# Optimization experiments

Hardware: AMD Instinct MI355X
Metric: run time of the kernel (lower is better)

Reference implementation:

```python
import jax, jax.numpy as jnp
import numpy as np

EPS = 1e-5
N_KNN = 16


def _knn_idx(query_feat, ref_feat, k):
    # query_feat: (B, N, C), ref_feat: (B, M, C) -> idx (B, N, k) of smallest sq-dist
    q2 = jnp.sum(query_feat * query_feat, axis=-1, keepdims=True)        # (B,N,1)
    r2 = jnp.sum(ref_feat * ref_feat, axis=-1)[:, None, :]               # (B,1,M)
    d = q2 + r2 - 2.0 * jnp.einsum('bnc,bmc->bnm', query_feat, ref_feat)  # (B,N,M)
    _, idx = jax.lax.top_k(-d, k)
    return idx


def _group(x, idx):
    # x: (B, C, M), idx: (B, N, k) -> (B, C, N, k)
    B, C, M = x.shape
    _, N, k = idx.shape
    flat = jnp.broadcast_to(idx.reshape(B, 1, N * k), (B, C, N * k))
    return jnp.take_along_axis(x, flat, axis=2).reshape(B, C, N, k)


def _bn(x, g, b, m, v):
    # eval-mode BatchNorm2d over channel axis 1 of (B,C,N,k)
    inv = g / jnp.sqrt(v + EPS)
    return x * inv[None, :, None, None] + (b - m * inv)[None, :, None, None]


def setup_inputs() -> dict:
    key = jax.random.key(0)
    ks = jax.random.split(key, 24)
    B, C, N, N2 = 4, 256, 2048, 2048
    ph = 64  # pos_hidden_dim
    ah = 256  # dim * attn_hidden_multiplier = 64*4
    s = lambda fan: 1.0 / np.sqrt(fan)
    inp = {
        'pcd': jax.random.normal(ks[0], (B, 3, N), jnp.float32),
        'feat': jax.random.normal(ks[1], (B, C, N), jnp.float32),
        'pcd_feadb': jax.random.normal(ks[2], (B, 3, N2), jnp.float32),
        'feat_feadb': jax.random.normal(ks[3], (B, C, N2), jnp.float32),
        'pos_w1': jax.random.normal(ks[4], (ph, 3), jnp.float32) * s(3),
        'pos_b1': jax.random.normal(ks[5], (ph,), jnp.float32) * 0.01,
        'pos_g': jax.random.uniform(ks[6], (ph,), jnp.float32, 0.5, 1.5),
        'pos_be': jax.random.normal(ks[7], (ph,), jnp.float32) * 0.01,
        'pos_m': jax.random.normal(ks[8], (ph,), jnp.float32) * 0.1,
        'pos_v': jax.random.uniform(ks[9], (ph,), jnp.float32, 0.5, 1.5),
        'pos_w2': jax.random.normal(ks[10], (C, ph), jnp.float32) * s(ph),
        'pos_b2': jax.random.normal(ks[11], (C,), jnp.float32) * 0.01,
        'attn_w1': jax.random.normal(ks[12], (ah, C), jnp.float32) * s(C),
        'attn_b1': jax.random.normal(ks[13], (ah,), jnp.float32) * 0.01,
        'attn_g': jax.random.uniform(ks[14], (ah,), jnp.float32, 0.5, 1.5),
        'attn_be': jax.random.normal(ks[15], (ah,), jnp.float32) * 0.01,
        'attn_m': jax.random.normal(ks[16], (ah,), jnp.float32) * 0.1,
        'attn_v': jax.random.uniform(ks[17], (ah,), jnp.float32, 0.5, 1.5),
        'attn_w2': jax.random.normal(ks[18], (C, ah), jnp.float32) * s(ah),
        'attn_b2': jax.random.normal(ks[19], (C,), jnp.float32) * 0.01,
    }
    return inp


def reference(pcd, feat, pcd_feadb, feat_feadb,
              pos_w1, pos_b1, pos_g, pos_be, pos_m, pos_v, pos_w2, pos_b2,
              attn_w1, attn_b1, attn_g, attn_be, attn_m, attn_v, attn_w2, attn_b2):
    fusion_pcd = jnp.concatenate([pcd, pcd_feadb], axis=2)    # (B,3,M)
    fusion_feat = jnp.concatenate([feat, feat_feadb], axis=2)  # (B,C,M)
    # KNN in feature space: neighbors of each key point among fusion set
    idx = _knn_idx(jnp.swapaxes(feat, 1, 2), jnp.swapaxes(fusion_feat, 1, 2), N_KNN)  # (B,N,k)
    group_point = _group(fusion_pcd, idx)   # (B,3,N,k)
    group_feat = _group(fusion_feat, idx)   # (B,C,N,k)
    qk_rel = feat[:, :, :, None] - group_feat
    pos_rel = pcd[:, :, :, None] - group_point
    # pos_mlp: conv1x1 -> BN -> relu -> conv1x1
    h = jnp.einsum('oc,bcnk->bonk', pos_w1, pos_rel) + pos_b1[None, :, None, None]
    h = jax.nn.relu(_bn(h, pos_g, pos_be, pos_m, pos_v))
    pos_embedding = jnp.einsum('oc,bcnk->bonk', pos_w2, h) + pos_b2[None, :, None, None]
    # attn_mlp
    a = jnp.einsum('oc,bcnk->bonk', attn_w1, qk_rel + pos_embedding) + attn_b1[None, :, None, None]
    a = jax.nn.relu(_bn(a, attn_g, attn_be, attn_m, attn_v))
    a = jnp.einsum('oc,bcnk->bonk', attn_w2, a) + attn_b2[None, :, None, None]
    sample_weight = jax.nn.softmax(a, axis=-1)  # softmax over the k neighbors
    refined_feat = jnp.sum(sample_weight * (group_feat + pos_embedding), axis=-1)  # (B,C,N)
    return refined_feat
```

## Files before the change

### kernel.cpp

```cpp
#include <hip/hip_runtime.h>
#include <float.h>

#define CDIM 256
#define NPTS 2048
#define MPTS 4096
#define NB   4
#define KNN  16
#define COLS 64
#define NCHUNK 8
#define CSIZE  512
#define NSTEPS 16
#define QPB   128

typedef _Float16 half8 __attribute__((ext_vector_type(8)));
typedef _Float16 half4 __attribute__((ext_vector_type(4)));
typedef float    f32x4 __attribute__((ext_vector_type(4)));

__device__ __forceinline__ int swzS(int row, int byte) {
    return row * 512 + (byte ^ ((row & 7) << 4));
}
__device__ __forceinline__ int swz128(int row, int byte) {
    return row * 128 + (byte ^ ((row & 7) << 4));
}

__device__ __forceinline__ float sum16(float v) {
    v += __uint_as_float(__builtin_amdgcn_update_dpp(0, __float_as_uint(v), 0x128, 0xF, 0xF, true));
    v += __uint_as_float(__builtin_amdgcn_update_dpp(0, __float_as_uint(v), 0x124, 0xF, 0xF, true));
    v += __uint_as_float(__builtin_amdgcn_update_dpp(0, __float_as_uint(v), 0x122, 0xF, 0xF, true));
    v += __uint_as_float(__builtin_amdgcn_update_dpp(0, __float_as_uint(v), 0x121, 0xF, 0xF, true));
    return v;
}

#define CEA(x, y)                                                               \
    { unsigned lo_ = kk[x] < kk[y] ? kk[x] : kk[y];                             \
      unsigned hi_ = kk[x] < kk[y] ? kk[y] : kk[x];                             \
      kk[x] = lo_; kk[y] = hi_; }
#define CED(x, y)                                                               \
    { unsigned hi_ = td[x] > td[y] ? td[x] : td[y];                             \
      unsigned lo_ = td[x] > td[y] ? td[y] : td[x];                             \
      td[x] = hi_; td[y] = lo_; }
#define RESORT16                                                                \
    CED(0,8) CED(1,9) CED(2,10) CED(3,11) CED(4,12) CED(5,13) CED(6,14) CED(7,15) \
    CED(0,4) CED(1,5) CED(2,6) CED(3,7) CED(8,12) CED(9,13) CED(10,14) CED(11,15) \
    CED(0,2) CED(1,3) CED(4,6) CED(5,7) CED(8,10) CED(9,11) CED(12,14) CED(13,15) \
    CED(0,1) CED(2,3) CED(4,5) CED(6,7) CED(8,9) CED(10,11) CED(12,13) CED(14,15)

__global__ __launch_bounds__(256) void tposeHL2(const float* __restrict__ feat,
                                                const float* __restrict__ featdb,
                                                _Float16* __restrict__ featH,
                                                _Float16* __restrict__ featL,
                                                float* __restrict__ r2) {
    __shared__ float red[8][33];
    const int b = blockIdx.y;
    const int mt = blockIdx.x;
    const int m = threadIdx.x & 31;
    const int cp = threadIdx.x >> 5;
    const int mg = mt * 32 + m;
    const float* src = (mg < NPTS) ? (feat + (size_t)b * CDIM * NPTS + mg)
                                   : (featdb + (size_t)b * CDIM * NPTS + (mg - NPTS));
    const int c0 = cp * 32;
    float acc = 0.f;
    half8 hh[4], ll[4];
#pragma unroll
    for (int i = 0; i < 32; i++) {
        float v = src[(size_t)(c0 + i) * NPTS];
        acc += v * v;
        _Float16 h = (_Float16)v;
        hh[i >> 3][i & 7] = h;
        ll[i >> 3][i & 7] = (_Float16)(v - (float)h);
    }
    _Float16* dh = featH + ((size_t)b * MPTS + mg) * CDIM + c0;
    _Float16* dl = featL + ((size_t)b * MPTS + mg) * CDIM + c0;
#pragma unroll
    for (int i = 0; i < 4; i++) {
        *(half8*)(dh + i * 8) = hh[i];
        *(half8*)(dl + i * 8) = ll[i];
    }
    red[cp][m] = acc;
    __syncthreads();
    if (threadIdx.x < 32) {
        float s = 0.f;
#pragma unroll
        for (int j = 0; j < 8; j++) s += red[j][threadIdx.x];
        r2[b * MPTS + mt * 32 + threadIdx.x] = s;
    }
}

__global__ __launch_bounds__(256) void wcvt(const float* __restrict__ aw1,
                                            const float* __restrict__ aw2,
                                            const float* __restrict__ pw2,
                                            _Float16* __restrict__ aw1h,
                                            _Float16* __restrict__ aw2h,
                                            _Float16* __restrict__ pw2h) {
    int i = blockIdx.x * 256 + threadIdx.x;
    if (i < 65536) { aw1h[i] = (_Float16)aw1[i]; aw2h[i] = (_Float16)aw2[i]; }
    if (i < 16384) { pw2h[i] = (_Float16)pw2[i]; }
}

__global__ __launch_bounds__(512, 4) void score_knn(const _Float16* __restrict__ featH,
                                                    const _Float16* __restrict__ featL,
                                                    const float* __restrict__ r2g,
                                                    unsigned* __restrict__ partial) {
    __shared__ __align__(16) char sbuf[65536];
    __shared__ float sr2[CSIZE];

    const int tid = threadIdx.x;
    const int lane = tid & 63, wave = tid >> 6;
    const int l15 = lane & 15, l4 = lane >> 4;
    const int chunk = blockIdx.x, qt = blockIdx.y, b = blockIdx.z;
    const int nq = qt * QPB + wave * 16 + l15;
    const int m0 = chunk * CSIZE;

    sr2[tid] = r2g[b * MPTS + m0 + tid];

    half8 qh[8], ql[8];
    {
        const _Float16* qb = featH + ((size_t)b * MPTS + nq) * CDIM + l4 * 8;
        const _Float16* qL = featL + ((size_t)b * MPTS + nq) * CDIM + l4 * 8;
#pragma unroll
        for (int ks = 0; ks < 8; ks++) {
            qh[ks] = *(const half8*)(qb + ks * 32);
            ql[ks] = *(const half8*)(qL + ks * 32);
        }
    }

    int adr[8];
#pragma unroll
    for (int ks = 0; ks < 8; ks++)
        adr[ks] = (ks * 4 + l4) * 512 + ((l15 * 16) ^ ((ks & 7) << 4));

    const int srow = tid >> 4;
    const int o0 = 2 * (tid & 15);
    int wadr[2];
#pragma unroll
    for (int j = 0; j < 2; j++) {
        int o = o0 + j;
        wadr[j] = o * 512 + ((srow * 16) ^ (((o >> 2) & 7) << 4));
    }
    const char* gH = (const char*)(featH + ((size_t)b * MPTS + m0 + srow) * CDIM) + o0 * 16;
    const char* gL = (const char*)(featL + ((size_t)b * MPTS + m0 + srow) * CDIM) + o0 * 16;

    unsigned td[16];
#pragma unroll
    for (int i = 0; i < 16; i++) td[i] = 0xFFFFFFFFu;

    half8 pH[2], pL[2];
#pragma unroll
    for (int j = 0; j < 2; j++) {
        pH[j] = *(const half8*)(gH + j * 16);
        pL[j] = *(const half8*)(gL + j * 16);
    }
    gH += 32 * CDIM * 2;
    gL += 32 * CDIM * 2;

    for (int s = 0; s < NSTEPS; ++s) {
        char* buf = sbuf + (s & 1) * 32768;
#pragma unroll
        for (int j = 0; j < 2; j++) {
            *(half8*)(buf + wadr[j])         = pH[j];
            *(half8*)(buf + 16384 + wadr[j]) = pL[j];
        }
        __syncthreads();

        if (s < NSTEPS - 1) {
#pragma unroll
            for (int j = 0; j < 2; j++) {
                pH[j] = *(const half8*)(gH + j * 16);
                pL[j] = *(const half8*)(gL + j * 16);
            }
            gH += 32 * CDIM * 2;
            gL += 32 * CDIM * 2;
        }

        unsigned kk[8];
#pragma unroll
        for (int sub = 0; sub < 2; ++sub) {
            f32x4 a0 = {0.f, 0.f, 0.f, 0.f};
            f32x4 a1 = {0.f, 0.f, 0.f, 0.f};
            f32x4 a2 = {0.f, 0.f, 0.f, 0.f};
#pragma unroll
            for (int ks = 0; ks < 8; ks++) {
                half8 ah = *(const half8*)(buf + adr[ks] + sub * 256);
                half8 al = *(const half8*)(buf + 16384 + adr[ks] + sub * 256);
                a0 = __builtin_amdgcn_mfma_f32_16x16x32_f16(ah, qh[ks], a0, 0, 0, 0);
                a1 = __builtin_amdgcn_mfma_f32_16x16x32_f16(ah, ql[ks], a1, 0, 0, 0);
                a2 = __builtin_amdgcn_mfma_f32_16x16x32_f16(al, qh[ks], a2, 0, 0, 0);
            }
            float4 s4 = *(const float4*)(sr2 + s * 32 + sub * 16 + 4 * l4);
            const float sv[4] = {s4.x, s4.y, s4.z, s4.w};
            const int mloc0 = s * 32 + sub * 16 + 4 * l4;
#pragma unroll
            for (int r = 0; r < 4; r++) {
                float d = fmaxf(sv[r] - 2.f * (a0[r] + a1[r] + a2[r]), 0.f);
                unsigned dq = (unsigned)(d * 4096.f);
                dq = dq > 0x7FFFF0u ? 0x7FFFF0u : dq;
                kk[sub * 4 + r] = (dq << 9) | (unsigned)(mloc0 + r);
            }
        }
        CEA(0,1) CEA(2,3) CEA(4,5) CEA(6,7)
        CEA(0,2) CEA(1,3) CEA(4,6) CEA(5,7)
        CEA(1,2) CEA(5,6) CEA(0,4) CEA(3,7)
        CEA(1,5) CEA(2,6)
        CEA(1,4) CEA(3,6)
        CEA(2,4) CEA(3,5)
        CEA(3,4)
#pragma unroll
        for (int i = 0; i < 8; i++) td[i] = td[i] < kk[i] ? td[i] : kk[i];
        RESORT16
    }

#pragma unroll
    for (int rr = 0; rr < 2; rr++) {
        const int dx = 16 << rr;
        unsigned ot[16];
#pragma unroll
        for (int e = 0; e < 16; e++) ot[e] = __shfl_xor(td[e], dx);
#pragma unroll
        for (int e = 0; e < 16; e++) {
            unsigned o = ot[15 - e];
            td[e] = td[e] < o ? td[e] : o;
        }
        RESORT16
    }
    if (l4 == 0) {
        const size_t qrow = (size_t)b * NPTS + qt * QPB + wave * 16 + l15;
#pragma unroll
        for (int e = 0; e < 16; e++)
            partial[(size_t)(chunk * 16 + e) * (NB * NPTS) + qrow] = td[e];
    }
}

__global__ __launch_bounds__(256) void merge16(const unsigned* __restrict__ partial,
                                               int* __restrict__ idxout) {
    const int row = blockIdx.x * 256 + threadIdx.x;
    unsigned long long td[16];
#pragma unroll
    for (int i = 0; i < 16; i++) td[i] = 0x8000000000ull + (unsigned long long)i;
    unsigned long long curmax = 0x800000000Full;
    for (int e = 0; e < NCHUNK * 16; e++) {
        unsigned k = partial[(size_t)e * (NB * NPTS) + row];
        unsigned long long k64 =
            (((unsigned long long)(k >> 9)) << 12) |
            (unsigned long long)((unsigned)((e >> 4) << 9) | (k & 0x1FFu));
        if (k64 < curmax) {
#pragma unroll
            for (int i_ = 0; i_ < 16; i_++) td[i_] = (td[i_] == curmax) ? k64 : td[i_];
            unsigned long long nm_ = td[0];
#pragma unroll
            for (int i_ = 1; i_ < 16; i_++) nm_ = td[i_] > nm_ ? td[i_] : nm_;
            curmax = nm_;
        }
    }
#pragma unroll
    for (int e = 0; e < 16; e++) idxout[row * 16 + e] = (int)(td[e] & 0xFFFull);
}

__global__ __launch_bounds__(512, 4) void fused_mlp6(
    const float* __restrict__ pcd, const float* __restrict__ pcddb,
    const _Float16* __restrict__ featH, const int* __restrict__ knn,
    const float* __restrict__ pw1, const float* __restrict__ pb1,
    const float* __restrict__ pg, const float* __restrict__ pbe,
    const float* __restrict__ pm, const float* __restrict__ pv,
    const _Float16* __restrict__ pw2h, const float* __restrict__ pb2,
    const _Float16* __restrict__ aw1h, const float* __restrict__ ab1,
    const float* __restrict__ ag, const float* __restrict__ abe,
    const float* __restrict__ am, const float* __restrict__ av,
    const _Float16* __restrict__ aw2h,
    float* __restrict__ out) {
    __shared__ __align__(16) _Float16 xbuf[COLS * 256];
    __shared__ __align__(16) _Float16 hbuf[COLS * 64];
    __shared__ __align__(16) float pr[3][COLS];
    __shared__ int sidx[COLS];
    __shared__ __align__(16) float ainv[256], ash2[256], pinv[64], psh[64];

    const int tid = threadIdx.x;
    const int lane = tid & 63, wave = tid >> 6;
    const int l15 = lane & 15, l4 = lane >> 4;
    const int blk = blockIdx.x;
    const int b = blk >> 9;
    const int n0 = (blk & 511) * 4;
    const int R0 = wave * 32;

    if (tid < COLS) {
        sidx[tid] = knn[(size_t)(b * NPTS + n0 + (tid >> 4)) * KNN + (tid & 15)];
    } else if (tid < COLS + 256) {
        int c = tid - COLS;
        float inv = ag[c] / sqrtf(av[c] + 1e-5f);
        ainv[c] = inv;
        ash2[c] = abe[c] - am[c] * inv + ab1[c] * inv;
    } else if (tid < COLS + 256 + 64) {
        int o = tid - COLS - 256;
        float inv = pg[o] / sqrtf(pv[o] + 1e-5f);
        pinv[o] = inv;
        psh[o] = pbe[o] - pm[o] * inv;
    }
    half8 wp[2][2];
#pragma unroll
    for (int rt = 0; rt < 2; rt++)
#pragma unroll
        for (int ks = 0; ks < 2; ks++)
            wp[rt][ks] = *(const half8*)(pw2h + (size_t)(R0 + rt * 16 + l15) * 64 +
                                         ks * 32 + l4 * 8);
    __syncthreads();

    if (tid < 3 * COLS) {
        int c = tid >> 6, col = tid & 63;
        int m = sidx[col];
        const float* pc = pcd + ((size_t)b * 3 + c) * NPTS;
        const float* px = pcddb + ((size_t)b * 3 + c) * NPTS;
        float gp = (m < NPTS) ? pc[m] : px[m - NPTS];
        pr[c][col] = pc[n0 + (col >> 4)] - gp;
    }
    const int colx = tid & 63;
    const int c0x = (tid >> 6) * 32;
    half8 fmv[4], fnv[4];
    {
        const _Float16* fmp = featH + ((size_t)b * MPTS + sidx[colx]) * CDIM + c0x;
        const _Float16* fnp = featH + ((size_t)b * MPTS + n0 + (colx >> 4)) * CDIM + c0x;
#pragma unroll
        for (int j = 0; j < 4; j++) {
            fmv[j] = *(const half8*)(fmp + j * 8);
            fnv[j] = *(const half8*)(fnp + j * 8);
        }
    }
    __syncthreads();

    {
        int col = tid >> 3, o0 = (tid & 7) * 8;
        float x0 = pr[0][col], x1 = pr[1][col], x2 = pr[2][col];
        half8 hv;
#pragma unroll
        for (int i = 0; i < 8; i++) {
            int o = o0 + i;
            float v = pw1[o * 3] * x0 + pw1[o * 3 + 1] * x1 + pw1[o * 3 + 2] * x2 + pb1[o];
            v = fmaxf(v * pinv[o] + psh[o], 0.f);
            hv[i] = (_Float16)v;
        }
        *(half8*)((char*)hbuf + swz128(col, o0 * 2)) = hv;
    }
    __syncthreads();

    f32x4 acc[2][4];
#pragma unroll
    for (int rt = 0; rt < 2; rt++)
#pragma unroll
        for (int ct = 0; ct < 4; ct++) acc[rt][ct] = (f32x4){0.f, 0.f, 0.f, 0.f};
#pragma unroll
    for (int ks = 0; ks < 2; ks++) {
        int k0 = ks * 32 + l4 * 8;
#pragma unroll
        for (int ct = 0; ct < 4; ct++) {
            half8 bb = *(const half8*)((char*)hbuf + swz128(ct * 16 + l15, k0 * 2));
            acc[0][ct] = __builtin_amdgcn_mfma_f32_16x16x32_f16(wp[0][ks], bb, acc[0][ct], 0, 0, 0);
            acc[1][ct] = __builtin_amdgcn_mfma_f32_16x16x32_f16(wp[1][ks], bb, acc[1][ct], 0, 0, 0);
        }
    }
    half4 pe4[2][4];
#pragma unroll
    for (int rt = 0; rt < 2; rt++) {
        int cb = R0 + rt * 16 + 4 * l4;
        float4 pb = *(const float4*)(pb2 + cb);
        float pbv[4] = {pb.x, pb.y, pb.z, pb.w};
#pragma unroll
        for (int ct = 0; ct < 4; ct++) {
            int col = ct * 16 + l15;
            half4 p4;
#pragma unroll
            for (int r = 0; r < 4; r++) p4[r] = (_Float16)(acc[rt][ct][r] + pbv[r]);
            pe4[rt][ct] = p4;
            *(half4*)((char*)xbuf + swzS(col, cb * 2)) = p4;
        }
    }
    __syncthreads();

#pragma unroll
    for (int j = 0; j < 4; j++) {
        int c = c0x + j * 8;
        half8 vp = *(const half8*)((char*)xbuf + swzS(colx, c * 2));
        half8 xv = fnv[j] - fmv[j] + vp;
        *(half8*)((char*)xbuf + swzS(colx, c * 2)) = xv;
    }
    half8 wa[8];
#pragma unroll
    for (int ks = 0; ks < 8; ks++)
        wa[ks] = *(const half8*)(aw1h + (size_t)(R0 + l15) * 256 + ks * 32 + l4 * 8);
    __syncthreads();

#pragma unroll
    for (int rt = 0; rt < 2; rt++)
#pragma unroll
        for (int ct = 0; ct < 4; ct++) acc[rt][ct] = (f32x4){0.f, 0.f, 0.f, 0.f};
#pragma unroll
    for (int ks = 0; ks < 8; ks++) {
        int k0 = ks * 32 + l4 * 8;
#pragma unroll
        for (int ct = 0; ct < 4; ct++) {
            half8 bb = *(const half8*)((char*)xbuf + swzS(ct * 16 + l15, k0 * 2));
            acc[0][ct] = __builtin_amdgcn_mfma_f32_16x16x32_f16(wa[ks], bb, acc[0][ct], 0, 0, 0);
        }
    }
#pragma unroll
    for (int ks = 0; ks < 8; ks++)
        wa[ks] = *(const half8*)(aw1h + (size_t)(R0 + 16 + l15) * 256 + ks * 32 + l4 * 8);
#pragma unroll
    for (int ks = 0; ks < 8; ks++) {
        int k0 = ks * 32 + l4 * 8;
#pragma unroll
        for (int ct = 0; ct < 4; ct++) {
            half8 bb = *(const half8*)((char*)xbuf + swzS(ct * 16 + l15, k0 * 2));
            acc[1][ct] = __builtin_amdgcn_mfma_f32_16x16x32_f16(wa[ks], bb, acc[1][ct], 0, 0, 0);
        }
    }
    __syncthreads();

#pragma unroll
    for (int rt = 0; rt < 2; rt++) {
        int cb = R0 + rt * 16 + 4 * l4;
        float4 iv = *(const float4*)(&ainv[cb]);
        float4 sh = *(const float4*)(&ash2[cb]);
        float ivv[4] = {iv.x, iv.y, iv.z, iv.w};
        float shv[4] = {sh.x, sh.y, sh.z, sh.w};
#pragma unroll
        for (int ct = 0; ct < 4; ct++) {
            int col = ct * 16 + l15;
            half4 h4;
#pragma unroll
            for (int r = 0; r < 4; r++)
                h4[r] = (_Float16)fmaxf(acc[rt][ct][r] * ivv[r] + shv[r], 0.f);
            *(half4*)((char*)xbuf + swzS(col, cb * 2)) = h4;
        }
    }
#pragma unroll
    for (int ks = 0; ks < 8; ks++)
        wa[ks] = *(const half8*)(aw2h + (size_t)(R0 + l15) * 256 + ks * 32 + l4 * 8);
    __syncthreads();

#pragma unroll
    for (int rt = 0; rt < 2; rt++)
#pragma unroll
        for (int ct = 0; ct < 4; ct++) acc[rt][ct] = (f32x4){0.f, 0.f, 0.f, 0.f};
#pragma unroll
    for (int ks = 0; ks < 8; ks++) {
        int k0 = ks * 32 + l4 * 8;
#pragma unroll
        for (int ct = 0; ct < 4; ct++) {
            half8 bb = *(const half8*)((char*)xbuf + swzS(ct * 16 + l15, k0 * 2));
            acc[0][ct] = __builtin_amdgcn_mfma_f32_16x16x32_f16(wa[ks], bb, acc[0][ct], 0, 0, 0);
        }
    }
#pragma unroll
    for (int ks = 0; ks < 8; ks++)
        wa[ks] = *(const half8*)(aw2h + (size_t)(R0 + 16 + l15) * 256 + ks * 32 + l4 * 8);
#pragma unroll
    for (int ks = 0; ks < 8; ks++) {
        int k0 = ks * 32 + l4 * 8;
#pragma unroll
        for (int ct = 0; ct < 4; ct++) {
            half8 bb = *(const half8*)((char*)xbuf + swzS(ct * 16 + l15, k0 * 2));
            acc[1][ct] = __builtin_amdgcn_mfma_f32_16x16x32_f16(wa[ks], bb, acc[1][ct], 0, 0, 0);
        }
    }

#pragma unroll
    for (int rt = 0; rt < 2; rt++) {
        int cb = R0 + rt * 16 + 4 * l4;
        half4 gfa[4];
#pragma unroll
        for (int ct = 0; ct < 4; ct++)
            gfa[ct] = *(const half4*)(featH +
                ((size_t)b * MPTS + sidx[ct * 16 + l15]) * CDIM + cb);
#pragma unroll
        for (int ct = 0; ct < 4; ct++) {
            float oo[4], ss[4];
#pragma unroll
            for (int r = 0; r < 4; r++) {
                float v = acc[rt][ct][r];
                v = fminf(fmaxf(v, -60.f), 60.f);
                float e = __expf(v);
                float sv = (float)gfa[ct][r] + (float)pe4[rt][ct][r];
                ss[r] = sum16(e);
                oo[r] = sum16(e * sv);
            }
            if (l15 < 4) {
                float o = l15 == 0 ? oo[0] : l15 == 1 ? oo[1] : l15 == 2 ? oo[2] : oo[3];
                float s = l15 == 0 ? ss[0] : l15 == 1 ? ss[1] : l15 == 2 ? ss[2] : ss[3];
                out[((size_t)b * CDIM + cb + l15) * NPTS + n0 + ct] =
                    o * __builtin_amdgcn_rcpf(s);
            }
        }
    }
}

extern "C" void kernel_launch(void* const* d_in, const int* in_sizes, int n_in,
                              void* d_out, int out_size, void* d_ws, size_t ws_size,
                              hipStream_t stream) {
    const float* pcd    = (const float*)d_in[0];
    const float* feat   = (const float*)d_in[1];
    const float* pcddb  = (const float*)d_in[2];
    const float* featdb = (const float*)d_in[3];
    const float* pw1 = (const float*)d_in[4];
    const float* pb1 = (const float*)d_in[5];
    const float* pg  = (const float*)d_in[6];
    const float* pbe = (const float*)d_in[7];
    const float* pm  = (const float*)d_in[8];
    const float* pv  = (const float*)d_in[9];
    const float* pw2 = (const float*)d_in[10];
    const float* pb2 = (const float*)d_in[11];
    const float* aw1 = (const float*)d_in[12];
    const float* ab1 = (const float*)d_in[13];
    const float* ag  = (const float*)d_in[14];
    const float* abe = (const float*)d_in[15];
    const float* am  = (const float*)d_in[16];
    const float* av  = (const float*)d_in[17];
    const float* aw2 = (const float*)d_in[18];
    float* out = (float*)d_out;

    char* ws = (char*)d_ws;
    _Float16* featH   = (_Float16*)(ws);
    _Float16* featL   = (_Float16*)(ws + 8388608);
    float*    ws_r2   = (float*)(ws + 16777216);
    unsigned* partial = (unsigned*)(ws + 16842752);
    int*      ws_idx  = (int*)(ws + 21037056);
    _Float16* aw1h    = (_Float16*)(ws + 21561344);
    _Float16* aw2h    = (_Float16*)(ws + 21692416);
    _Float16* pw2h    = (_Float16*)(ws + 21823488);

    wcvt<<<256, 256, 0, stream>>>(aw1, aw2, pw2, aw1h, aw2h, pw2h);
    tposeHL2<<<dim3(MPTS / 32, NB), 256, 0, stream>>>(feat, featdb, featH, featL, ws_r2);
    score_knn<<<dim3(NCHUNK, NPTS / QPB, NB), 512, 0, stream>>>(featH, featL, ws_r2, partial);
    merge16<<<NB * NPTS / 256, 256, 0, stream>>>(partial, ws_idx);
    fused_mlp6<<<NB * (NPTS / 4), 512, 0, stream>>>(
        pcd, pcddb, featH, ws_idx,
        pw1, pb1, pg, pbe, pm, pv, pw2h, pb2,
        aw1h, ab1, ag, abe, am, av, aw2h, out);
}
```

Baseline: 272.4 us.

## Double queries per score_knn block to halve reference-tile reloads

Raises queries per block from 128 to 256 and launches 1024-thread blocks, so each staged reference chunk in shared memory serves twice as many query waves. Each thread now loads one half8 per step instead of two, and the r2 shared-memory fill is guarded for the larger block. This halves the global reads of the reference features and the number of blocks. In exchange, fewer blocks fit per CU, each barrier has to sync 16 waves, and there are fewer blocks overall to fill the GPU.

After: 266.9 us. 2.0% less time.

```diff
diff --git a/kernel.cpp b/kernel.cpp
--- a/kernel.cpp
+++ b/kernel.cpp
@@ -10,7 +10,7 @@
 #define NCHUNK 8
 #define CSIZE  512
 #define NSTEPS 16
-#define QPB   128
+#define QPB   256
 
 typedef _Float16 half8 __attribute__((ext_vector_type(8)));
 typedef _Float16 half4 __attribute__((ext_vector_type(4)));
@@ -97,10 +97,10 @@
     if (i < 16384) { pw2h[i] = (_Float16)pw2[i]; }
 }
 
-__global__ __launch_bounds__(512, 4) void score_knn(const _Float16* __restrict__ featH,
-                                                    const _Float16* __restrict__ featL,
-                                                    const float* __restrict__ r2g,
-                                                    unsigned* __restrict__ partial) {
+__global__ __launch_bounds__(1024, 2) void score_knn(const _Float16* __restrict__ featH,
+                                                     const _Float16* __restrict__ featL,
+                                                     const float* __restrict__ r2g,
+                                                     unsigned* __restrict__ partial) {
     __shared__ __align__(16) char sbuf[65536];
     __shared__ float sr2[CSIZE];
 
@@ -111,7 +111,7 @@
     const int nq = qt * QPB + wave * 16 + l15;
     const int m0 = chunk * CSIZE;
 
-    sr2[tid] = r2g[b * MPTS + m0 + tid];
+    if (tid < CSIZE) sr2[tid] = r2g[b * MPTS + m0 + tid];
 
     half8 qh[8], ql[8];
     {
@@ -129,45 +129,30 @@
     for (int ks = 0; ks < 8; ks++)
         adr[ks] = (ks * 4 + l4) * 512 + ((l15 * 16) ^ ((ks & 7) << 4));
 
-    const int srow = tid >> 4;
-    const int o0 = 2 * (tid & 15);
-    int wadr[2];
-#pragma unroll
-    for (int j = 0; j < 2; j++) {
-        int o = o0 + j;
-        wadr[j] = o * 512 + ((srow * 16) ^ (((o >> 2) & 7) << 4));
-    }
-    const char* gH = (const char*)(featH + ((size_t)b * MPTS + m0 + srow) * CDIM) + o0 * 16;
-    const char* gL = (const char*)(featL + ((size_t)b * MPTS + m0 + srow) * CDIM) + o0 * 16;
+    const int srow = tid >> 5;
+    const int oo = tid & 31;
+    const int wadr = oo * 512 + ((srow * 16) ^ (((oo >> 2) & 7) << 4));
+    const char* gH = (const char*)(featH + ((size_t)b * MPTS + m0 + srow) * CDIM) + oo * 16;
+    const char* gL = (const char*)(featL + ((size_t)b * MPTS + m0 + srow) * CDIM) + oo * 16;
 
     unsigned td[16];
 #pragma unroll
     for (int i = 0; i < 16; i++) td[i] = 0xFFFFFFFFu;
 
-    half8 pH[2], pL[2];
-#pragma unroll
-    for (int j = 0; j < 2; j++) {
-        pH[j] = *(const half8*)(gH + j * 16);
-        pL[j] = *(const half8*)(gL + j * 16);
-    }
+    half8 pH = *(const half8*)gH;
+    half8 pL = *(const half8*)gL;
     gH += 32 * CDIM * 2;
     gL += 32 * CDIM * 2;
 
     for (int s = 0; s < NSTEPS; ++s) {
         char* buf = sbuf + (s & 1) * 32768;
-#pragma unroll
-        for (int j = 0; j < 2; j++) {
-            *(half8*)(buf + wadr[j])         = pH[j];
-            *(half8*)(buf + 16384 + wadr[j]) = pL[j];
-        }
+        *(half8*)(buf + wadr)         = pH;
+        *(half8*)(buf + 16384 + wadr) = pL;
         __syncthreads();
 
         if (s < NSTEPS - 1) {
-#pragma unroll
-            for (int j = 0; j < 2; j++) {
-                pH[j] = *(const half8*)(gH + j * 16);
-                pL[j] = *(const half8*)(gL + j * 16);
-            }
+            pH = *(const half8*)gH;
+            pL = *(const half8*)gL;
             gH += 32 * CDIM * 2;
             gL += 32 * CDIM * 2;
         }
@@ -527,7 +512,7 @@
 
     wcvt<<<256, 256, 0, stream>>>(aw1, aw2, pw2, aw1h, aw2h, pw2h);
     tposeHL2<<<dim3(MPTS / 32, NB), 256, 0, stream>>>(feat, featdb, featH, featL, ws_r2);
-    score_knn<<<dim3(NCHUNK, NPTS / QPB, NB), 512, 0, stream>>>(featH, featL, ws_r2, partial);
+    score_knn<<<dim3(NCHUNK, NPTS / QPB, NB), 1024, 0, stream>>>(featH, featL, ws_r2, partial);
     merge16<<<NB * NPTS / 256, 256, 0, stream>>>(partial, ws_idx);
     fused_mlp6<<<NB * (NPTS / 4), 512, 0, stream>>>(
         pcd, pcddb, featH, ws_idx,
```
